# Kernel optimization log

Measured on AMD Instinct MI355X. Metric: run time of the kernel, lower is better.

The kernel has to match this reference:

```python
import jax, jax.numpy as jnp
import numpy as np

B, L, WORD, H = 16, 32, 512, 1024
HALF = H // 2
TEMP = 1.0


def setup_inputs() -> dict:
    key = jax.random.key(0)
    ks = jax.random.split(key, 12)
    sd = 0.05
    f32 = jnp.float32
    # torch LSTMCell combined bias with forget-gate bias = 1 (gate order i,f,g,o)
    b_lstm = jnp.concatenate([jnp.zeros(HALF), jnp.ones(HALF), jnp.zeros(2 * HALF)]).astype(f32)
    return {
        "sentence_embedding": jax.random.normal(ks[0], (B, L, WORD), f32),
        "length": jax.random.randint(ks[1], (B,), L // 2, L + 1),
        "W_ih_f": jax.random.normal(ks[2], (4 * HALF, WORD), f32) * sd,
        "W_hh_f": jax.random.normal(ks[3], (4 * HALF, HALF), f32) * sd,
        "b_f": b_lstm,
        "W_ih_b": jax.random.normal(ks[4], (4 * HALF, WORD), f32) * sd,
        "W_hh_b": jax.random.normal(ks[5], (4 * HALF, HALF), f32) * sd,
        "b_b": b_lstm,
        "W_rank1": jax.random.normal(ks[6], (256, WORD + 1), f32) * sd,
        "W_rank2": jax.random.normal(ks[7], (1, 256), f32) * sd,
        "W_comp": jax.random.normal(ks[8], (5 * H, 3 * H), f32) * 0.02,
        "b_comp": jnp.zeros((5 * H,), f32),
    }


def _lstm(xs, W_ih, W_hh, b):
    # xs: (L, B, D) -> hs, cs: (B, L, HALF); torch LSTMCell gate order i,f,g,o
    n = xs.shape[1]
    hdim = W_hh.shape[1]

    def step(carry, xt):
        h, c = carry
        g = xt @ W_ih.T + h @ W_hh.T + b
        i, f, gg, o = jnp.split(g, 4, axis=1)
        c = jax.nn.sigmoid(f) * c + jax.nn.sigmoid(i) * jnp.tanh(gg)
        h = jax.nn.sigmoid(o) * jnp.tanh(c)
        return (h, c), (h, c)

    init = (jnp.zeros((n, hdim), xs.dtype), jnp.zeros((n, hdim), xs.dtype))
    _, (hs, cs) = jax.lax.scan(step, init, xs)
    return hs.transpose(1, 0, 2), cs.transpose(1, 0, 2)


def _rev_padded(x, lengths):
    # reverse the first lengths[b] timesteps of each sequence, keep padding in place
    t = np.arange(x.shape[1])
    idx = np.where(t[None, :] < lengths[:, None], lengths[:, None] - 1 - t[None, :], t[None, :])
    return jnp.take_along_axis(x, jnp.asarray(idx)[:, :, None], axis=1)


def _rank_score(seg, W1, W2):
    l = seg.shape[0]
    pos = (2.0 * jnp.arange(l, dtype=seg.dtype) / l - 1.0)[:, None]
    xy = jnp.concatenate([seg, pos], axis=1)
    return jax.nn.relu(xy @ W1.T) @ W2.T  # (l, 1)


def _compose(lst, rst, xst, Wc, bc):
    # Nary tree-LSTM composition over (left, right, current) states; None -> zeros
    hx, cx = xst
    zero = jnp.zeros_like(hx)
    hl, cl = lst if lst is not None else (zero, zero)
    hr, cr = rst if rst is not None else (zero, zero)
    g = jnp.concatenate([hl, hr, hx], axis=1) @ Wc.T + bc  # (1, 5H)
    i, fl, fr, u, o = jnp.split(g, 5, axis=1)
    c = jax.nn.sigmoid(fl) * cl + jax.nn.sigmoid(fr) * cr + jax.nn.sigmoid(i) * jnp.tanh(u)
    h = jax.nn.sigmoid(o) * jnp.tanh(c)
    return h, c


def _build(emb, hs, cs, start, end, W1, W2, Wc, bc, sent, splits, record):
    if end == start:
        return None
    if end == start + 1:
        return (hs[start:start + 1], cs[start:start + 1])
    logits_t = _rank_score(emb[start:end], W1, W2).T  # (1, l)
    y_soft = jax.nn.softmax(logits_t / TEMP, axis=1)
    if record:
        k = int(jnp.argmax(y_soft[0]))
        splits[(sent, start, end)] = k
    else:
        k = splits[(sent, start, end)]
    hard = jnp.zeros_like(y_soft).at[0, k].set(1.0)
    gate = jax.lax.stop_gradient(hard - y_soft) + y_soft  # straight-through estimator
    h = gate @ hs[start:end]
    c = gate @ cs[start:end]
    pos = start + k
    left = _build(emb, hs, cs, start, pos, W1, W2, Wc, bc, sent, splits, record)
    right = _build(emb, hs, cs, pos + 1, end, W1, W2, Wc, bc, sent, splits, record)
    return _compose(left, right, (h, c), Wc, bc)


def _forward(sentence_embedding, length, W_ih_f, W_hh_f, b_f, W_ih_b, W_hh_b, b_b,
             W_rank1, W_rank2, W_comp, b_comp, splits, record):
    lengths = np.asarray(length)
    hs_f, cs_f = _lstm(sentence_embedding.transpose(1, 0, 2), W_ih_f, W_hh_f, b_f)
    x_bw = _rev_padded(sentence_embedding, lengths)
    hs_b, cs_b = _lstm(x_bw.transpose(1, 0, 2), W_ih_b, W_hh_b, b_b)
    hs_b = _rev_padded(hs_b, lengths)
    cs_b = _rev_padded(cs_b, lengths)
    hs = jnp.concatenate([hs_f, hs_b], axis=2)  # (B, L, H)
    cs = jnp.concatenate([cs_f, cs_b], axis=2)
    h_out, c_out = [], []
    for i in range(sentence_embedding.shape[0]):
        st = _build(sentence_embedding[i], hs[i], cs[i], 0, int(lengths[i]),
                    W_rank1, W_rank2, W_comp, b_comp, i, splits, record)
        h_out.append(st[0])
        c_out.append(st[1])
    return jnp.concatenate(h_out, axis=0), jnp.concatenate(c_out, axis=0)


def reference(sentence_embedding, length, W_ih_f, W_hh_f, b_f, W_ih_b, W_hh_b, b_b,
              W_rank1, W_rank2, W_comp, b_comp):
    return _forward(sentence_embedding, length, W_ih_f, W_hh_f, b_f,
                    W_ih_b, W_hh_b, b_b, W_rank1, W_rank2, W_comp, b_comp, {}, True)
```

## Files before the change

kernel.cpp:

```cpp
#include <hip/hip_runtime.h>
#include <math.h>

#define NB 16
#define SL 32
#define H5 5120
#define K3 3072

typedef __attribute__((ext_vector_type(8))) short short8;
typedef __attribute__((ext_vector_type(4))) float floatx4;
typedef __attribute__((ext_vector_type(4))) int intx4;

__device__ __forceinline__ float sigf(float x) { return 1.0f / (1.0f + expf(-x)); }

__device__ __forceinline__ unsigned short f2bf(float x) {
  union { float f; unsigned int u; } v;
  v.f = x;
  unsigned int r = v.u + 0x7FFFu + ((v.u >> 16) & 1u);
  return (unsigned short)(r >> 16);
}


__device__ __forceinline__ void bar32(int* flags, int idx, int mygen) {
  asm volatile("s_waitcnt vmcnt(0)" ::: "memory");
  __syncthreads();
  const int tid = threadIdx.x;
  if (tid == 0)
    __hip_atomic_store(&flags[idx], mygen, __ATOMIC_RELAXED,
                       __HIP_MEMORY_SCOPE_AGENT);
  if (tid < 64) {
    const int off = (tid & 7) * 4;
    int ok;
    do {
      intx4 f;
      asm volatile("global_load_dwordx4 %0, %1, off sc0 sc1\n\t"
                   "s_waitcnt vmcnt(0)"
                   : "=&v"(f) : "v"(flags + off) : "memory");
      ok = (f.x >= mygen) & (f.y >= mygen) & (f.z >= mygen) & (f.w >= mygen);
    } while (__all(ok) == 0);
  }
  __syncthreads();
}

__device__ __forceinline__ void bar512(int* flags, int idx, int mygen) {
  asm volatile("s_waitcnt vmcnt(0)" ::: "memory");
  __syncthreads();
  const int tid = threadIdx.x;
  if (tid == 0)
    __hip_atomic_store(&flags[idx], mygen, __ATOMIC_RELAXED,
                       __HIP_MEMORY_SCOPE_AGENT);
  if (tid < 64) {
    int ok;
    do {
      intx4 f0, f1;
      asm volatile("global_load_dwordx4 %0, %2, off sc0 sc1\n\t"
                   "global_load_dwordx4 %1, %3, off sc0 sc1\n\t"
                   "s_waitcnt vmcnt(0)"
                   : "=&v"(f0), "=&v"(f1)
                   : "v"(flags + tid * 8), "v"(flags + tid * 8 + 4)
                   : "memory");
      ok = (f0.x >= mygen) & (f0.y >= mygen) & (f0.z >= mygen) & (f0.w >= mygen)
         & (f1.x >= mygen) & (f1.y >= mygen) & (f1.z >= mygen) & (f1.w >= mygen);
    } while (__all(ok) == 0);
  }
  __syncthreads();
}


__global__ void k_zero(float* __restrict__ p, int n) {
  int i = blockIdx.x * blockDim.x + threadIdx.x;
  if (i < n) p[i] = 0.0f;
}

__global__ void k_conv6(const float* s0, unsigned short* d0, int n0,
                        const float* s1, unsigned short* d1, int n1,
                        const float* s2, unsigned short* d2, int n2,
                        const float* s3, unsigned short* d3, int n3,
                        const float* s4, unsigned short* d4, int n4,
                        const float* s5, unsigned short* d5, int n5)
{
  const float* s; unsigned short* d; int n;
  switch (blockIdx.y) {
    case 0: s = s0; d = d0; n = n0; break;
    case 1: s = s1; d = d1; n = n1; break;
    case 2: s = s2; d = d2; n = n2; break;
    case 3: s = s3; d = d3; n = n3; break;
    case 4: s = s4; d = d4; n = n4; break;
    default: s = s5; d = d5; n = n5; break;
  }
  const int nf4 = n >> 2;
  for (int i = blockIdx.x * blockDim.x + threadIdx.x; i < nf4; i += gridDim.x * blockDim.x) {
    const float4 v = *(const float4*)&s[i * 4];
    ushort4 o;
    o.x = f2bf(v.x); o.y = f2bf(v.y); o.z = f2bf(v.z); o.w = f2bf(v.w);
    *(ushort4*)&d[i * 4] = o;
  }
}

__global__ __launch_bounds__(256)
void k_gemm(const float* __restrict__ A, int lda,
            const float* __restrict__ W, int ldw,
            float* __restrict__ out, int N, int K)
{
  __shared__ __align__(16) float sm[2 * 16 * 68];
  float* As = sm;
  float* Ws = sm + 16 * 68;
  const int tid = threadIdx.x;
  const int tx = tid & 15, ty = tid >> 4;
  const int g0 = blockIdx.x * 64, r0 = blockIdx.y * 64;
  float acc[4][4];
#pragma unroll
  for (int i = 0; i < 4; ++i)
#pragma unroll
    for (int j = 0; j < 4; ++j) acc[i][j] = 0.0f;
  const int ks = tid & 15, rr = tid >> 4;
  for (int kt = 0; kt < K; kt += 16) {
#pragma unroll
    for (int rep = 0; rep < 4; ++rep) {
      As[ks * 68 + rep * 16 + rr] = A[(size_t)(r0 + rep * 16 + rr) * lda + kt + ks];
      Ws[ks * 68 + rep * 16 + rr] = W[(size_t)(g0 + rep * 16 + rr) * ldw + kt + ks];
    }
    __syncthreads();
#pragma unroll
    for (int k = 0; k < 16; ++k) {
      const float4 a4 = *(const float4*)&As[k * 68 + ty * 4];
      const float4 w4 = *(const float4*)&Ws[k * 68 + tx * 4];
      const float av[4] = {a4.x, a4.y, a4.z, a4.w};
      const float wv[4] = {w4.x, w4.y, w4.z, w4.w};
#pragma unroll
      for (int i = 0; i < 4; ++i)
#pragma unroll
        for (int j = 0; j < 4; ++j) acc[i][j] += av[i] * wv[j];
    }
    __syncthreads();
  }
#pragma unroll
  for (int i = 0; i < 4; ++i) {
    const int r = r0 + ty * 4 + i;
    float4 o;
    o.x = acc[i][0]; o.y = acc[i][1]; o.z = acc[i][2]; o.w = acc[i][3];
    *(float4*)&out[(size_t)r * N + g0 + tx * 4] = o;
  }
}

__global__ __launch_bounds__(256)
void k_xproj(const unsigned short* __restrict__ embB,
             const unsigned short* __restrict__ WfB, const unsigned short* __restrict__ WbB,
             float* __restrict__ Xf, float* __restrict__ Xb)
{
  const unsigned short* B = blockIdx.z ? WbB : WfB;
  float* out = blockIdx.z ? Xb : Xf;
  __shared__ __align__(16) unsigned short As[128 * 40];
  __shared__ __align__(16) unsigned short Bs[128 * 40];
  const int tid = threadIdx.x;
  const int g0 = blockIdx.x * 128;
  const int r0 = blockIdx.y * 128;
  const int wave = tid >> 6, lane = tid & 63;
  const int wm = wave >> 1, wn = wave & 1;
  const int l15 = lane & 15, quad = lane >> 4;
  floatx4 acc[4][4];
#pragma unroll
  for (int mt = 0; mt < 4; ++mt)
#pragma unroll
    for (int nt = 0; nt < 4; ++nt) acc[mt][nt] = (floatx4){0.f, 0.f, 0.f, 0.f};
  for (int kt = 0; kt < 512; kt += 32) {
    __syncthreads();
#pragma unroll
    for (int p = 0; p < 2; ++p) {
      const int i = tid + p * 256;
      const int row = i >> 2, q = i & 3;
      *(uint4*)&As[row * 40 + q * 8] = *(const uint4*)&embB[(size_t)(r0 + row) * 512 + kt + q * 8];
      *(uint4*)&Bs[row * 40 + q * 8] = *(const uint4*)&B[(size_t)(g0 + row) * 512 + kt + q * 8];
    }
    __syncthreads();
    short8 af[4], bfr[4];
#pragma unroll
    for (int mt = 0; mt < 4; ++mt)
      af[mt] = *(const short8*)&As[(wm * 64 + mt * 16 + l15) * 40 + quad * 8];
#pragma unroll
    for (int nt = 0; nt < 4; ++nt)
      bfr[nt] = *(const short8*)&Bs[(wn * 64 + nt * 16 + l15) * 40 + quad * 8];
#pragma unroll
    for (int mt = 0; mt < 4; ++mt)
#pragma unroll
      for (int nt = 0; nt < 4; ++nt)
        acc[mt][nt] = __builtin_amdgcn_mfma_f32_16x16x32_bf16(af[mt], bfr[nt], acc[mt][nt], 0, 0, 0);
  }
#pragma unroll
  for (int nt = 0; nt < 4; ++nt) {
    const int col = g0 + wn * 64 + nt * 16 + l15;
#pragma unroll
    for (int mt = 0; mt < 4; ++mt)
#pragma unroll
      for (int i = 0; i < 4; ++i) {
        const int row = r0 + wm * 64 + mt * 16 + quad * 4 + i;
        out[(size_t)row * 2048 + col] = acc[mt][nt][i];
      }
  }
}

__global__ __launch_bounds__(256)
void k_mfma_gemm(const unsigned short* __restrict__ U, const unsigned short* __restrict__ WcB,
                 const float* __restrict__ bc, float* __restrict__ gB)
{
  __shared__ __align__(16) unsigned short As[128 * 40];
  __shared__ __align__(16) unsigned short Bs[64 * 40];
  const int bid = blockIdx.x;
  const int r0 = (bid / 80) * 128;
  const int g0 = (bid % 80) * 64;
  const int tid = threadIdx.x;
  const int wave = tid >> 6, lane = tid & 63;
  const int wm = wave >> 1, wn = wave & 1;
  const int l15 = lane & 15, quad = lane >> 4;
  floatx4 acc[4][2];
#pragma unroll
  for (int mf = 0; mf < 4; ++mf)
#pragma unroll
    for (int nt = 0; nt < 2; ++nt) acc[mf][nt] = (floatx4){0.f, 0.f, 0.f, 0.f};
  const int a_row = tid >> 2, a_q = tid & 3;
  for (int kt = 0; kt < K3; kt += 32) {
    __syncthreads();
#pragma unroll
    for (int p = 0; p < 2; ++p) {
      const int i = tid + p * 256;
      const int row = i >> 2, q = i & 3;
      *(uint4*)&As[row * 40 + q * 8] = *(const uint4*)&U[(size_t)(r0 + row) * K3 + kt + q * 8];
    }
    *(uint4*)&Bs[a_row * 40 + a_q * 8] = *(const uint4*)&WcB[(size_t)(g0 + a_row) * K3 + kt + a_q * 8];
    __syncthreads();
    short8 af[4], bfr[2];
#pragma unroll
    for (int mf = 0; mf < 4; ++mf)
      af[mf] = *(const short8*)&As[(wm * 64 + mf * 16 + l15) * 40 + quad * 8];
#pragma unroll
    for (int nt = 0; nt < 2; ++nt)
      bfr[nt] = *(const short8*)&Bs[(wn * 32 + nt * 16 + l15) * 40 + quad * 8];
#pragma unroll
    for (int mf = 0; mf < 4; ++mf)
#pragma unroll
      for (int nt = 0; nt < 2; ++nt)
        acc[mf][nt] = __builtin_amdgcn_mfma_f32_16x16x32_bf16(af[mf], bfr[nt], acc[mf][nt], 0, 0, 0);
  }
#pragma unroll
  for (int nt = 0; nt < 2; ++nt) {
    const int col = g0 + wn * 32 + nt * 16 + l15;
    const float bias = bc[col];
#pragma unroll
    for (int mf = 0; mf < 4; ++mf)
#pragma unroll
      for (int i = 0; i < 4; ++i) {
        const int row = r0 + wm * 64 + mf * 16 + quad * 4 + i;
        gB[(size_t)row * H5 + col] = acc[mf][nt][i] + bias;
      }
  }
}

__global__ __launch_bounds__(256)
void k_scan(const float* __restrict__ Xf, const float* __restrict__ Xb,
            const unsigned short* __restrict__ WhfB, const unsigned short* __restrict__ WhbB,
            const float* __restrict__ bf, const float* __restrict__ bb,
            const int* __restrict__ len,
            unsigned short* __restrict__ hbB, float* __restrict__ cbuf,
            float* __restrict__ hs, float* __restrict__ cs, int* __restrict__ bar)
{
  const int bid = blockIdx.x;
  const int dir = bid >> 5;
  const int hjt = bid & 31;
  const int tid = threadIdx.x;
  const int wave = tid >> 6, lane = tid & 63;
  const int l15 = lane & 15, quad = lane >> 4;
  const unsigned short* Wh = dir ? WhbB : WhfB;
  const float* bias = dir ? bb : bf;
  const float* X = dir ? Xb : Xf;
  int* myflags = &bar[512 + dir * 32];
  __shared__ float sg[4 * 16 * 17];
  const int jg = wave * 512 + hjt * 16 + l15;
  short8 wfr[16];
#pragma unroll
  for (int k8 = 0; k8 < 16; ++k8)
    wfr[k8] = *(const short8*)&Wh[(size_t)jg * 512 + k8 * 32 + quad * 8];
  const int bb_ = tid >> 4, j = tid & 15;
  const int hj = hjt * 16 + j;
  const int Lb = len[bb_];
  const float bi_i = bias[hj];
  const float bi_f = bias[512 + hj];
  const float bi_g = bias[1024 + hj];
  const float bi_o = bias[1536 + hj];
  for (int t = 0; t < SL; ++t) {
    const int pp = t & 1;
    const unsigned short* hp = hbB + (size_t)(dir * 2 + pp) * 8192;
    unsigned short* hn = hbB + (size_t)(dir * 2 + (pp ^ 1)) * 8192;
    const float* cp = cbuf + (size_t)(dir * 2 + pp) * 8192;
    float* cn = cbuf + (size_t)(dir * 2 + (pp ^ 1)) * 8192;
    int xidx = t;
    if (dir) xidx = (t < Lb) ? (Lb - 1 - t) : t;
    const float* xr = X + (size_t)(bb_ * SL + xidx) * 2048;
    const float x0 = xr[hj];
    const float x1 = xr[512 + hj];
    const float x2 = xr[1024 + hj];
    const float x3 = xr[1536 + hj];
    const float cprev = cp[bb_ * 512 + hj];
    short8 afr[16];
#pragma unroll
    for (int k8 = 0; k8 < 16; ++k8)
      asm volatile("global_load_dwordx4 %0, %1, off sc0 sc1"
                   : "=&v"(afr[k8])
                   : "v"(&hp[(size_t)l15 * 512 + k8 * 32 + quad * 8]));
    asm volatile("s_waitcnt vmcnt(0)" ::: "memory");
    __builtin_amdgcn_sched_barrier(0);
    floatx4 acc = (floatx4){0.f, 0.f, 0.f, 0.f};
#pragma unroll
    for (int k8 = 0; k8 < 16; ++k8)
      acc = __builtin_amdgcn_mfma_f32_16x16x32_bf16(afr[k8], wfr[k8], acc, 0, 0, 0);
#pragma unroll
    for (int i = 0; i < 4; ++i)
      sg[wave * 272 + (quad * 4 + i) * 17 + l15] = acc[i];
    __syncthreads();
    const float gi = sg[0 * 272 + bb_ * 17 + j] + x0 + bi_i;
    const float gf = sg[1 * 272 + bb_ * 17 + j] + x1 + bi_f;
    const float gg = sg[2 * 272 + bb_ * 17 + j] + x2 + bi_g;
    const float go = sg[3 * 272 + bb_ * 17 + j] + x3 + bi_o;
    const float cnew = sigf(gf) * cprev + sigf(gi) * tanhf(gg);
    const float hnew = sigf(go) * tanhf(cnew);
    cn[bb_ * 512 + hj] = cnew;
    const unsigned int hb16 = f2bf(hnew);
    asm volatile("global_store_short %0, %1, off sc0 sc1"
                 :: "v"(&hn[bb_ * 512 + hj]), "v"(hb16) : "memory");
    const int pos = dir ? xidx : t;
    const int col = dir ? (512 + hj) : hj;
    hs[(size_t)(bb_ * SL + pos) * 1024 + col] = hnew;
    cs[(size_t)(bb_ * SL + pos) * 1024 + col] = cnew;
    if (t != SL - 1) bar32(myflags, hjt, t + 1);
  }
}

__global__ __launch_bounds__(256)
void k_score(const float* __restrict__ E1, const float* __restrict__ Wr1,
             const float* __restrict__ Wr2, const int* __restrict__ len,
             int* __restrict__ ksplit)
{
  const int b = blockIdx.x;
  const int s = blockIdx.y;
  const int L = len[b];
  if (s + 2 > L) return;
  const int tid = threadIdx.x;
  __shared__ float e[32 * 257];
  __shared__ float w1p[256];
  __shared__ float w2s[256];
  __shared__ float red[32 * 8];
  __shared__ float sc[32];
  const int nrow = 32 - s;
  for (int i = tid; i < nrow * 256; i += 256) {
    const int rr = i >> 8, q = i & 255;
    e[rr * 257 + q] = E1[(size_t)(b * SL + s + rr) * 256 + q];
  }
  w1p[tid] = Wr1[tid * 513 + 512];
  w2s[tid] = Wr2[tid];
  __syncthreads();
  const int t_ = tid & 31, jg = tid >> 5;
  const int lmax = L - s;
  for (int l = 2; l <= lmax; ++l) {
    float part = 0.0f;
    if (t_ < l) {
      const float pos = 2.0f * (float)t_ / (float)l - 1.0f;
      const float* er = e + t_ * 257;
      for (int q = jg * 32; q < jg * 32 + 32; ++q) {
        const float v = er[q] + pos * w1p[q];
        part += fmaxf(v, 0.0f) * w2s[q];
      }
    }
    red[t_ * 8 + jg] = part;
    __syncthreads();
    if (jg == 0 && t_ < l) {
      float su = 0.0f;
      for (int q = 0; q < 8; ++q) su += red[t_ * 8 + q];
      sc[t_] = su;
    }
    __syncthreads();
    if (tid == 0) {
      int k = 0;
      float best = sc[0];
      for (int q = 1; q < l; ++q)
        if (sc[q] > best) { best = sc[q]; k = q; }
      ksplit[(b * 32 + s) * 33 + l] = k;
    }
    __syncthreads();
  }
}

__global__ __launch_bounds__(64)
void k_walk(const int* __restrict__ ksplit, const int* __restrict__ len,
            int* __restrict__ meta)
{
  const int b = blockIdx.x;
  const int tid = threadIdx.x;
  __shared__ int ks[32 * 33];
  __shared__ int stk[96];
  for (int i = tid; i < 32 * 33; i += 64) ks[i] = ksplit[b * 1056 + i];
  __syncthreads();
  if (tid != 0) return;
  int* own = meta;
  int* lt = meta + 512;
  int* li = meta + 1024;
  int* rt = meta + 1536;
  int* ri = meta + 2048;
  int* dep = meta + 2560;
  int* nn = meta + 3072;
  int* dcnt = meta + 3088;
  int* lcnt = meta + 3120;
  int* dlist = meta + 3152;
  int* llist = meta + 19536;
  int sp = 0, nn_ = 1;
  stk[0] = 0; stk[1] = len[b]; stk[2] = 0;
  sp = 1;
  while (sp > 0) {
    sp--;
    const int s = stk[sp * 3], eN = stk[sp * 3 + 1], nid = stk[sp * 3 + 2];
    const int l = eN - s;
    const int k = ks[s * 33 + l];
    const int m = b * 32 + nid;
    own[m] = s + k;
    if (k == 0) { lt[m] = 0; li[m] = 0; }
    else if (k == 1) { lt[m] = 1; li[m] = s; }
    else {
      const int id = nn_++;
      lt[m] = 2; li[m] = id;
      stk[sp * 3] = s; stk[sp * 3 + 1] = s + k; stk[sp * 3 + 2] = id; sp++;
    }
    const int rl = l - k - 1;
    if (rl == 0) { rt[m] = 0; ri[m] = 0; }
    else if (rl == 1) { rt[m] = 1; ri[m] = s + k + 1; }
    else {
      const int id = nn_++;
      rt[m] = 2; ri[m] = id;
      stk[sp * 3] = s + k + 1; stk[sp * 3 + 1] = eN; stk[sp * 3 + 2] = id; sp++;
    }
  }
  nn[b] = nn_;
  for (int i = nn_ - 1; i >= 0; --i) {
    const int m = b * 32 + i;
    int d = 1;
    if (lt[m] == 2) d = max(d, dep[b * 32 + li[m]] + 1);
    if (rt[m] == 2) d = max(d, dep[b * 32 + ri[m]] + 1);
    dep[m] = d;
  }
  for (int i = 0; i < nn_; ++i) {
    const int m = b * 32 + i;
    const int r = dep[m];
    const int idx = atomicAdd(&dcnt[r], 1);
    dlist[r * 512 + idx] = m;
    if (lt[m] == 2 || rt[m] == 2) {
      const int lx = atomicAdd(&lcnt[r], 1);
      llist[r * 512 + lx] = m;
    }
  }
}

__global__ __launch_bounds__(256)
void k_ubuild(const float* __restrict__ hs, const int* __restrict__ meta,
              unsigned short* __restrict__ U)
{
  const int id = blockIdx.x, b = blockIdx.y;
  const int tid = threadIdx.x;
  const int* own = meta;
  const int* lt = meta + 512;
  const int* li = meta + 1024;
  const int* rt = meta + 1536;
  const int* ri = meta + 2048;
  const int* nn = meta + 3072;
  const int m = b * 32 + id;
  unsigned short* u = U + (size_t)m * K3;
  if (id >= nn[b]) {
    for (int i = tid; i < K3; i += 256) u[i] = 0;
    return;
  }
  const float* hl = (lt[m] == 1) ? hs + (size_t)(b * 32 + li[m]) * 1024 : nullptr;
  const float* hr = (rt[m] == 1) ? hs + (size_t)(b * 32 + ri[m]) * 1024 : nullptr;
  const float* hx = hs + (size_t)(b * 32 + own[m]) * 1024;
  for (int i = tid; i < 1024; i += 256) {
    u[i] = hl ? f2bf(hl[i]) : 0;
    u[1024 + i] = hr ? f2bf(hr[i]) : 0;
    u[2048 + i] = f2bf(hx[i]);
  }
}

__global__ __launch_bounds__(256, 2)
void k_rounds(const unsigned short* __restrict__ WcB, const int* __restrict__ meta,
              unsigned short* __restrict__ nodehb,
              const float* __restrict__ gB, const float* __restrict__ cs,
              float* __restrict__ nodec,
              float* __restrict__ out, int* __restrict__ bar,
              const unsigned short* __restrict__ zpad)
{
  const int* lt = meta + 512;
  const int* li = meta + 1024;
  const int* rt = meta + 1536;
  const int* ri = meta + 2048;
  const int* dcnt = meta + 3088;
  const int* dlist = meta + 3152;
  __shared__ float scratch[4][16][16];
  __shared__ float gates[16][16];
  const int tid = threadIdx.x;
  const int bid = blockIdx.x;
  const int wave = tid >> 6, lane = tid & 63;
  const int l15 = lane & 15, quad = lane >> 4;
  const int j0 = bid * 2;
  const int cc = (l15 < 10) ? l15 : l15 - 10;
  const size_t wrow = (size_t)((cc >> 1) * 1024 + j0 + (cc & 1)) * K3;
  const int kbase = wave * 256 + quad * 8;
  short8 wreg[16];
#pragma unroll
  for (int i = 0; i < 8; ++i) {
    wreg[i]     = *(const short8*)&WcB[wrow + kbase + i * 32];
    wreg[8 + i] = *(const short8*)&WcB[wrow + 1024 + kbase + i * 32];
  }
  const int rnd = tid >> 4, rc = tid & 15;
  int bgen = 0;
  for (int r = 1; r <= 31; ++r) {
    const int cnt = dcnt[r];
    if (cnt == 0) break;
    if (r >= 2) { ++bgen; bar512(bar, bid, bgen); }
    for (int c0 = 0; c0 < cnt; c0 += 16) {
      float gBv = 0.0f;
      if (rc < 10 && c0 + rnd < cnt) {
        const int nodeP = dlist[r * 512 + c0 + rnd];
        gBv = gB[(size_t)nodeP * H5 + (rc >> 1) * 1024 + j0 + (rc & 1)];
      }
      const int ma = c0 + l15;
      const unsigned short* pl = zpad;
      const unsigned short* pr = zpad;
      if (ma < cnt) {
        const int node = dlist[r * 512 + ma];
        const int base = node & ~31;
        if (lt[node] == 2) pl = nodehb + (size_t)(base + li[node]) * 1024;
        if (rt[node] == 2) pr = nodehb + (size_t)(base + ri[node]) * 1024;
      }
      short8 al[8], ar[8];
#pragma unroll
      for (int i = 0; i < 8; ++i)
        asm volatile("global_load_dwordx4 %0, %1, off sc0 sc1"
                     : "=&v"(al[i]) : "v"(pl + kbase + i * 32));
#pragma unroll
      for (int i = 0; i < 8; ++i)
        asm volatile("global_load_dwordx4 %0, %1, off sc0 sc1"
                     : "=&v"(ar[i]) : "v"(pr + kbase + i * 32));
      floatx4 acc = (floatx4){0.f, 0.f, 0.f, 0.f};
      asm volatile("s_waitcnt vmcnt(8)" ::: "memory");
      __builtin_amdgcn_sched_barrier(0);
#pragma unroll
      for (int ks = 0; ks < 8; ++ks)
        acc = __builtin_amdgcn_mfma_f32_16x16x32_bf16(al[ks], wreg[ks], acc, 0, 0, 0);
      asm volatile("s_waitcnt vmcnt(0)" ::: "memory");
      __builtin_amdgcn_sched_barrier(0);
#pragma unroll
      for (int ks = 0; ks < 8; ++ks)
        acc = __builtin_amdgcn_mfma_f32_16x16x32_bf16(ar[ks], wreg[8 + ks], acc, 0, 0, 0);
      __syncthreads();
#pragma unroll
      for (int i = 0; i < 4; ++i)
        scratch[wave][quad * 4 + i][l15] = acc[i];
      __syncthreads();
      if (rc < 10)
        gates[rnd][rc] = gBv + scratch[0][rnd][rc] + scratch[1][rnd][rc]
                             + scratch[2][rnd][rc] + scratch[3][rnd][rc];
      __syncthreads();
      if (tid < 16) {
        const int mc = c0 + tid;
        if (mc < cnt) {
          const int node = dlist[r * 512 + mc];
          const int base = node & ~31;
          const int ltv = lt[node], rtv = rt[node];
          const float* clp = (ltv == 2) ? &nodec[(size_t)(base + li[node]) * 1024]
                           : (ltv == 1) ? &cs[(size_t)(base + li[node]) * 1024] : nullptr;
          const float* crp = (rtv == 2) ? &nodec[(size_t)(base + ri[node]) * 1024]
                           : (rtv == 1) ? &cs[(size_t)(base + ri[node]) * 1024] : nullptr;
          unsigned int pk = 0;
#pragma unroll
          for (int jj = 0; jj < 2; ++jj) {
            const int j = j0 + jj;
            const float gi  = gates[tid][0 + jj];
            const float gfl = gates[tid][2 + jj];
            const float gfr = gates[tid][4 + jj];
            const float gu  = gates[tid][6 + jj];
            const float go  = gates[tid][8 + jj];
            const float cl = clp ? clp[j] : 0.0f;
            const float cr = crp ? crp[j] : 0.0f;
            const float c_ = sigf(gfl) * cl + sigf(gfr) * cr + sigf(gi) * tanhf(gu);
            const float h  = sigf(go) * tanhf(c_);
            nodec[(size_t)node * 1024 + j] = c_;
            pk |= ((unsigned int)f2bf(h)) << (16 * jj);
            if ((node & 31) == 0) {
              const int b = node >> 5;
              out[b * 1024 + j] = h;
              out[16384 + b * 1024 + j] = c_;
            }
          }
          asm volatile("global_store_dword %0, %1, off sc0 sc1"
                       :: "v"(nodehb + (size_t)node * 1024 + j0), "v"(pk)
                       : "memory");
        }
      }
    }
  }
}

extern "C" void kernel_launch(void* const* d_in, const int* in_sizes, int n_in,
                              void* d_out, int out_size, void* d_ws, size_t ws_size,
                              hipStream_t stream) {
  const float* emb = (const float*)d_in[0];
  const int* len = (const int*)d_in[1];
  const float* Wihf = (const float*)d_in[2];
  const float* Whhf = (const float*)d_in[3];
  const float* bf = (const float*)d_in[4];
  const float* Wihb = (const float*)d_in[5];
  const float* Whhb = (const float*)d_in[6];
  const float* bb = (const float*)d_in[7];
  const float* Wr1 = (const float*)d_in[8];
  const float* Wr2 = (const float*)d_in[9];
  const float* Wc = (const float*)d_in[10];
  const float* bc = (const float*)d_in[11];
  float* out = (float*)d_out;

  float* ws = (float*)d_ws;
  float* Xf = ws;
  float* Xb = Xf + 1048576;
  float* hs = Xb + 1048576;
  float* cs = hs + 524288;
  float* E1 = cs + 524288;
  unsigned short* U = (unsigned short*)(E1 + 131072);
  float* gB = (float*)U + 786432;
  float* nodeh = gB + 2621440;
  float* nodec = nodeh + 524288;
  unsigned short* nodehb = (unsigned short*)(nodec + 524288);
  float* cbuf = (float*)nodehb + 262144;
  unsigned short* hbB = (unsigned short*)(cbuf + 32768);
  unsigned short* WcB = (unsigned short*)((float*)hbB + 16384);
  unsigned short* WihfB = WcB + 15728640;
  unsigned short* WihbB = WihfB + 1048576;
  unsigned short* WhhfB = WihbB + 1048576;
  unsigned short* WhhbB = WhhfB + 1048576;
  unsigned short* embB = WhhbB + 1048576;
  int* meta = (int*)(embB + 262144);
  int* ksplit = meta + 36096;
  int* bar = ksplit + 16896;
  unsigned short* zpad = (unsigned short*)(bar + 1024);

  k_zero<<<192, 256, 0, stream>>>(cbuf, 49152);
  k_zero<<<1, 64, 0, stream>>>((float*)(meta + 3088), 64);
  k_zero<<<6, 256, 0, stream>>>((float*)bar, 1536);
  k_conv6<<<dim3(1920, 6), 256, 0, stream>>>(
      Wc, WcB, 15728640, Wihf, WihfB, 1048576, Wihb, WihbB, 1048576,
      Whhf, WhhfB, 1048576, Whhb, WhhbB, 1048576, emb, embB, 262144);
  k_gemm<<<dim3(4, 8), 256, 0, stream>>>(emb, 512, Wr1, 513, E1, 256, 512);
  k_xproj<<<dim3(16, 4, 2), 256, 0, stream>>>(embB, WihfB, WihbB, Xf, Xb);
  k_scan<<<64, 256, 0, stream>>>(Xf, Xb, WhhfB, WhhbB, bf, bb, len, hbB,
                                 cbuf, hs, cs, bar);
  k_score<<<dim3(16, 31), 256, 0, stream>>>(E1, Wr1, Wr2, len, ksplit);
  k_walk<<<16, 64, 0, stream>>>(ksplit, len, meta);
  k_ubuild<<<dim3(32, 16), 256, 0, stream>>>(hs, meta, U);
  k_mfma_gemm<<<320, 256, 0, stream>>>(U, WcB, bc, gB);
  k_rounds<<<512, 256, 0, stream>>>(WcB, meta, nodehb, gB, cs,
                                    nodec, out, bar, zpad);
}
```

Before: 612.2 us.

## Merge launches, overlap scan with scoring, and use centralized barrier in rounds

```diff
diff --git a/kernel.cpp b/kernel.cpp
--- a/kernel.cpp
+++ b/kernel.cpp
@@ -18,7 +18,6 @@
   unsigned int r = v.u + 0x7FFFu + ((v.u >> 16) & 1u);
   return (unsigned short)(r >> 16);
 }
-
 
 __device__ __forceinline__ void bar32(int* flags, int idx, int mygen) {
   asm volatile("s_waitcnt vmcnt(0)" ::: "memory");
@@ -41,34 +40,46 @@
   __syncthreads();
 }
 
-__device__ __forceinline__ void bar512(int* flags, int idx, int mygen) {
+__device__ __forceinline__ void bar_rounds(int* flags, int* gen, int bid, int mygen) {
   asm volatile("s_waitcnt vmcnt(0)" ::: "memory");
   __syncthreads();
   const int tid = threadIdx.x;
-  if (tid == 0)
-    __hip_atomic_store(&flags[idx], mygen, __ATOMIC_RELAXED,
-                       __HIP_MEMORY_SCOPE_AGENT);
   if (tid < 64) {
-    int ok;
-    do {
-      intx4 f0, f1;
-      asm volatile("global_load_dwordx4 %0, %2, off sc0 sc1\n\t"
-                   "global_load_dwordx4 %1, %3, off sc0 sc1\n\t"
-                   "s_waitcnt vmcnt(0)"
-                   : "=&v"(f0), "=&v"(f1)
-                   : "v"(flags + tid * 8), "v"(flags + tid * 8 + 4)
-                   : "memory");
-      ok = (f0.x >= mygen) & (f0.y >= mygen) & (f0.z >= mygen) & (f0.w >= mygen)
-         & (f1.x >= mygen) & (f1.y >= mygen) & (f1.z >= mygen) & (f1.w >= mygen);
-    } while (__all(ok) == 0);
+    if (tid == 0)
+      __hip_atomic_store(&flags[bid], mygen, __ATOMIC_RELAXED,
+                         __HIP_MEMORY_SCOPE_AGENT);
+    if (bid == 0) {
+      int ok;
+      do {
+        intx4 f0, f1;
+        asm volatile("global_load_dwordx4 %0, %2, off sc0 sc1\n\t"
+                     "global_load_dwordx4 %1, %3, off sc0 sc1\n\t"
+                     "s_waitcnt vmcnt(0)"
+                     : "=&v"(f0), "=&v"(f1)
+                     : "v"(flags + tid * 8), "v"(flags + tid * 8 + 4)
+                     : "memory");
+        ok = (f0.x >= mygen) & (f0.y >= mygen) & (f0.z >= mygen) & (f0.w >= mygen)
+           & (f1.x >= mygen) & (f1.y >= mygen) & (f1.z >= mygen) & (f1.w >= mygen);
+      } while (__all(ok) == 0);
+      if (tid == 0)
+        __hip_atomic_store(gen, mygen, __ATOMIC_RELAXED,
+                           __HIP_MEMORY_SCOPE_AGENT);
+    } else if (tid == 0) {
+      while (__hip_atomic_load(gen, __ATOMIC_RELAXED,
+                               __HIP_MEMORY_SCOPE_AGENT) < mygen)
+        __builtin_amdgcn_s_sleep(2);
+    }
   }
   __syncthreads();
 }
 
 
-__global__ void k_zero(float* __restrict__ p, int n) {
+__global__ void k_zero3(float* a, int na, float* b, int nb_, float* c, int nc) {
+  const int stride = gridDim.x * blockDim.x;
   int i = blockIdx.x * blockDim.x + threadIdx.x;
-  if (i < n) p[i] = 0.0f;
+  for (int k = i; k < na; k += stride) a[k] = 0.0f;
+  for (int k = i; k < nb_; k += stride) b[k] = 0.0f;
+  for (int k = i; k < nc; k += stride) c[k] = 0.0f;
 }
 
 __global__ void k_conv6(const float* s0, unsigned short* d0, int n0,
@@ -96,28 +107,26 @@
   }
 }
 
-__global__ __launch_bounds__(256)
-void k_gemm(const float* __restrict__ A, int lda,
-            const float* __restrict__ W, int ldw,
-            float* __restrict__ out, int N, int K)
+__device__ void gemm_body(const float* __restrict__ A, const float* __restrict__ W,
+                          float* __restrict__ out, int bx, int by)
 {
   __shared__ __align__(16) float sm[2 * 16 * 68];
   float* As = sm;
   float* Ws = sm + 16 * 68;
   const int tid = threadIdx.x;
   const int tx = tid & 15, ty = tid >> 4;
-  const int g0 = blockIdx.x * 64, r0 = blockIdx.y * 64;
+  const int g0 = bx * 64, r0 = by * 64;
   float acc[4][4];
 #pragma unroll
   for (int i = 0; i < 4; ++i)
 #pragma unroll
     for (int j = 0; j < 4; ++j) acc[i][j] = 0.0f;
   const int ks = tid & 15, rr = tid >> 4;
-  for (int kt = 0; kt < K; kt += 16) {
+  for (int kt = 0; kt < 512; kt += 16) {
 #pragma unroll
     for (int rep = 0; rep < 4; ++rep) {
-      As[ks * 68 + rep * 16 + rr] = A[(size_t)(r0 + rep * 16 + rr) * lda + kt + ks];
-      Ws[ks * 68 + rep * 16 + rr] = W[(size_t)(g0 + rep * 16 + rr) * ldw + kt + ks];
+      As[ks * 68 + rep * 16 + rr] = A[(size_t)(r0 + rep * 16 + rr) * 512 + kt + ks];
+      Ws[ks * 68 + rep * 16 + rr] = W[(size_t)(g0 + rep * 16 + rr) * 513 + kt + ks];
     }
     __syncthreads();
 #pragma unroll
@@ -138,22 +147,19 @@
     const int r = r0 + ty * 4 + i;
     float4 o;
     o.x = acc[i][0]; o.y = acc[i][1]; o.z = acc[i][2]; o.w = acc[i][3];
-    *(float4*)&out[(size_t)r * N + g0 + tx * 4] = o;
-  }
-}
-
-__global__ __launch_bounds__(256)
-void k_xproj(const unsigned short* __restrict__ embB,
-             const unsigned short* __restrict__ WfB, const unsigned short* __restrict__ WbB,
-             float* __restrict__ Xf, float* __restrict__ Xb)
-{
-  const unsigned short* B = blockIdx.z ? WbB : WfB;
-  float* out = blockIdx.z ? Xb : Xf;
+    *(float4*)&out[(size_t)r * 256 + g0 + tx * 4] = o;
+  }
+}
+
+__device__ void xproj_body(const unsigned short* __restrict__ embB,
+                           const unsigned short* __restrict__ B,
+                           float* __restrict__ out, int bx, int by)
+{
   __shared__ __align__(16) unsigned short As[128 * 40];
   __shared__ __align__(16) unsigned short Bs[128 * 40];
   const int tid = threadIdx.x;
-  const int g0 = blockIdx.x * 128;
-  const int r0 = blockIdx.y * 128;
+  const int g0 = bx * 128;
+  const int r0 = by * 128;
   const int wave = tid >> 6, lane = tid & 63;
   const int wm = wave >> 1, wn = wave & 1;
   const int l15 = lane & 15, quad = lane >> 4;
@@ -199,6 +205,24 @@
 }
 
 __global__ __launch_bounds__(256)
+void k_proj(const float* __restrict__ emb, const float* __restrict__ Wr1,
+            float* __restrict__ E1,
+            const unsigned short* __restrict__ embB,
+            const unsigned short* __restrict__ WfB,
+            const unsigned short* __restrict__ WbB,
+            float* __restrict__ Xf, float* __restrict__ Xb)
+{
+  const int bid = blockIdx.x;
+  if (bid < 32) {
+    gemm_body(emb, Wr1, E1, bid & 3, bid >> 2);
+  } else {
+    const int idx = bid - 32;
+    const int bz = idx >> 6, rem = idx & 63;
+    xproj_body(embB, bz ? WbB : WfB, bz ? Xb : Xf, rem & 15, rem >> 4);
+  }
+}
+
+__global__ __launch_bounds__(256)
 void k_mfma_gemm(const unsigned short* __restrict__ U, const unsigned short* __restrict__ WcB,
                  const float* __restrict__ bc, float* __restrict__ gB)
 {
@@ -254,15 +278,15 @@
   }
 }
 
-__global__ __launch_bounds__(256)
-void k_scan(const float* __restrict__ Xf, const float* __restrict__ Xb,
-            const unsigned short* __restrict__ WhfB, const unsigned short* __restrict__ WhbB,
-            const float* __restrict__ bf, const float* __restrict__ bb,
-            const int* __restrict__ len,
-            unsigned short* __restrict__ hbB, float* __restrict__ cbuf,
-            float* __restrict__ hs, float* __restrict__ cs, int* __restrict__ bar)
-{
-  const int bid = blockIdx.x;
+__device__ void scan_body(const float* __restrict__ Xf, const float* __restrict__ Xb,
+                          const unsigned short* __restrict__ WhfB,
+                          const unsigned short* __restrict__ WhbB,
+                          const float* __restrict__ bf, const float* __restrict__ bb,
+                          const int* __restrict__ len,
+                          unsigned short* __restrict__ hbB, float* __restrict__ cbuf,
+                          float* __restrict__ hs, float* __restrict__ cs,
+                          int* __restrict__ bar, int bid)
+{
   const int dir = bid >> 5;
   const int hjt = bid & 31;
   const int tid = threadIdx.x;
@@ -271,7 +295,7 @@
   const unsigned short* Wh = dir ? WhbB : WhfB;
   const float* bias = dir ? bb : bf;
   const float* X = dir ? Xb : Xf;
-  int* myflags = &bar[512 + dir * 32];
+  int* myflags = &bar[528 + dir * 32];
   __shared__ float sg[4 * 16 * 17];
   const int jg = wave * 512 + hjt * 16 + l15;
   short8 wfr[16];
@@ -333,13 +357,10 @@
   }
 }
 
-__global__ __launch_bounds__(256)
-void k_score(const float* __restrict__ E1, const float* __restrict__ Wr1,
-             const float* __restrict__ Wr2, const int* __restrict__ len,
-             int* __restrict__ ksplit)
-{
-  const int b = blockIdx.x;
-  const int s = blockIdx.y;
+__device__ void score_body(const float* __restrict__ E1, const float* __restrict__ Wr1,
+                           const float* __restrict__ Wr2, const int* __restrict__ len,
+                           int* __restrict__ ksplit, int b, int s)
+{
   const int L = len[b];
   if (s + 2 > L) return;
   const int tid = threadIdx.x;
@@ -384,6 +405,22 @@
       ksplit[(b * 32 + s) * 33 + l] = k;
     }
     __syncthreads();
+  }
+}
+
+__global__ __launch_bounds__(256)
+void k_scansc(const float* Xf, const float* Xb,
+              const unsigned short* WhfB, const unsigned short* WhbB,
+              const float* bf, const float* bb, const int* len,
+              unsigned short* hbB, float* cbuf, float* hs, float* cs, int* bar,
+              const float* E1, const float* Wr1, const float* Wr2, int* ksplit)
+{
+  const int bid = blockIdx.x;
+  if (bid < 64) {
+    scan_body(Xf, Xb, WhfB, WhbB, bf, bb, len, hbB, cbuf, hs, cs, bar, bid);
+  } else {
+    const int idx = bid - 64;
+    score_body(E1, Wr1, Wr2, len, ksplit, idx / 31, idx % 31);
   }
 }
 
@@ -497,8 +534,8 @@
   const int* ri = meta + 2048;
   const int* dcnt = meta + 3088;
   const int* dlist = meta + 3152;
-  __shared__ float scratch[4][16][16];
-  __shared__ float gates[16][16];
+  __shared__ float scratch[4][16][17];
+  __shared__ float gates[16][17];
   const int tid = threadIdx.x;
   const int bid = blockIdx.x;
   const int wave = tid >> 6, lane = tid & 63;
@@ -518,7 +555,7 @@
   for (int r = 1; r <= 31; ++r) {
     const int cnt = dcnt[r];
     if (cnt == 0) break;
-    if (r >= 2) { ++bgen; bar512(bar, bid, bgen); }
+    if (r >= 2) { ++bgen; bar_rounds(bar, &bar[512], bid, bgen); }
     for (int c0 = 0; c0 < cnt; c0 += 16) {
       float gBv = 0.0f;
       if (rc < 10 && c0 + rnd < cnt) {
@@ -644,17 +681,14 @@
   int* bar = ksplit + 16896;
   unsigned short* zpad = (unsigned short*)(bar + 1024);
 
-  k_zero<<<192, 256, 0, stream>>>(cbuf, 49152);
-  k_zero<<<1, 64, 0, stream>>>((float*)(meta + 3088), 64);
-  k_zero<<<6, 256, 0, stream>>>((float*)bar, 1536);
+  k_zero3<<<128, 256, 0, stream>>>(cbuf, 49152, (float*)(meta + 3088), 64,
+                                   (float*)bar, 1536);
   k_conv6<<<dim3(1920, 6), 256, 0, stream>>>(
       Wc, WcB, 15728640, Wihf, WihfB, 1048576, Wihb, WihbB, 1048576,
       Whhf, WhhfB, 1048576, Whhb, WhhbB, 1048576, emb, embB, 262144);
-  k_gemm<<<dim3(4, 8), 256, 0, stream>>>(emb, 512, Wr1, 513, E1, 256, 512);
-  k_xproj<<<dim3(16, 4, 2), 256, 0, stream>>>(embB, WihfB, WihbB, Xf, Xb);
-  k_scan<<<64, 256, 0, stream>>>(Xf, Xb, WhhfB, WhhbB, bf, bb, len, hbB,
-                                 cbuf, hs, cs, bar);
-  k_score<<<dim3(16, 31), 256, 0, stream>>>(E1, Wr1, Wr2, len, ksplit);
+  k_proj<<<160, 256, 0, stream>>>(emb, Wr1, E1, embB, WihfB, WihbB, Xf, Xb);
+  k_scansc<<<560, 256, 0, stream>>>(Xf, Xb, WhhfB, WhhbB, bf, bb, len, hbB,
+                                    cbuf, hs, cs, bar, E1, Wr1, Wr2, ksplit);
   k_walk<<<16, 64, 0, stream>>>(ksplit, len, meta);
   k_ubuild<<<dim3(32, 16), 256, 0, stream>>>(hs, meta, U);
   k_mfma_gemm<<<320, 256, 0, stream>>>(U, WcB, bc, gB);
```

Result: faster. 550.1 us (-10.2%).
